# Kernel tuning notes

Hardware: AMD Instinct MI355X
Metric: run time of the kernel (lower is better)

## Reference

```python
import jax, jax.numpy as jnp
import numpy as np

B, S, D = 2, 2048, 1024
N_HEAD, D_ATTN = 16, 64


def setup_inputs() -> dict:
    key = jax.random.key(0)
    ks = jax.random.split(key, 5)
    x = jax.random.normal(ks[0], (B, S, D), dtype=jnp.float32)
    # causal mask: True = masked (as consumed by torch.masked_fill)
    mask = jnp.triu(jnp.ones((S, S), dtype=bool), k=1)
    scale = 0.02
    w_q = jax.random.normal(ks[1], (D, N_HEAD * D_ATTN), dtype=jnp.float32) * scale
    w_k = jax.random.normal(ks[2], (D, N_HEAD * D_ATTN), dtype=jnp.float32) * scale
    w_v = jax.random.normal(ks[3], (D, N_HEAD * D_ATTN), dtype=jnp.float32) * scale
    w_o = jax.random.normal(ks[4], (N_HEAD * D_ATTN, D), dtype=jnp.float32) * scale
    return {"x": x, "mask": mask, "w_q": w_q, "w_k": w_k, "w_v": w_v, "w_o": w_o}


def _split(t):
    # [B,S,H*Da] -> [B,H,S,Da]
    b, s, _ = t.shape
    return t.reshape(b, s, N_HEAD, D_ATTN).transpose(0, 2, 1, 3)


def reference(x, mask, w_q, w_k, w_v, w_o):
    q = _split(x @ w_q)
    k = _split(x @ w_k)
    v = _split(x @ w_v)
    scale = D_ATTN ** 0.5
    score = jnp.einsum("bhqd,bhkd->bhqk", q, k) / scale  # [B,H,S,S]
    score = jnp.where(mask, -jnp.inf, score)
    prob = jax.nn.softmax(score, axis=-1)
    out = jnp.einsum("bhqk,bhkd->bhqd", prob, v)
    out = out.transpose(0, 2, 1, 3).reshape(x.shape[0], x.shape[1], N_HEAD * D_ATTN)
    return out @ w_o
```

## Files before the change

kernel.cpp:

```cpp
#include <hip/hip_runtime.h>
#include <stdint.h>

using u16 = unsigned short;
using u32 = unsigned int;
using u64 = unsigned long long;

typedef float f32x4 __attribute__((ext_vector_type(4)));
typedef __bf16 bf16x8 __attribute__((ext_vector_type(8)));

#define DEV static __device__ __forceinline__

DEV u16 f2bf(float f) {
  u32 u = __float_as_uint(f);
  u += 0x7FFFu + ((u >> 16) & 1u);
  return (u16)(u >> 16);
}

DEV void gld16(const void* g, void* l) {
  __builtin_amdgcn_global_load_lds((__attribute__((address_space(1))) void*)g,
                                   (__attribute__((address_space(3))) void*)l,
                                   16, 0, 0);
}

__global__ void k_cvt_x(const float* __restrict__ x, u16* __restrict__ xb) {
  int i = (blockIdx.x * 256 + threadIdx.x) * 8;
  float4 a = *(const float4*)&x[i];
  float4 b = *(const float4*)&x[i + 4];
  __align__(16) u16 o[8];
  o[0] = f2bf(a.x); o[1] = f2bf(a.y); o[2] = f2bf(a.z); o[3] = f2bf(a.w);
  o[4] = f2bf(b.x); o[5] = f2bf(b.y); o[6] = f2bf(b.z); o[7] = f2bf(b.w);
  *(uint4*)&xb[i] = *(const uint4*)o;
}

__global__ void k_cvt_w(const float* __restrict__ w0, const float* __restrict__ w1,
                        const float* __restrict__ w2, const float* __restrict__ w3,
                        u16* __restrict__ t0, u16* __restrict__ t1,
                        u16* __restrict__ t2, u16* __restrict__ t3) {
  const float* w = blockIdx.z == 0 ? w0 : blockIdx.z == 1 ? w1 : blockIdx.z == 2 ? w2 : w3;
  u16* wt       = blockIdx.z == 0 ? t0 : blockIdx.z == 1 ? t1 : blockIdx.z == 2 ? t2 : t3;
  __shared__ __align__(16) float tile[64][68];
  const int tid = threadIdx.x;
  const int k0 = blockIdx.x * 64, n0 = blockIdx.y * 64;
#pragma unroll
  for (int i = 0; i < 4; ++i) {
    int c = tid + i * 256;
    int kr = c >> 4, col = (c & 15) * 4;
    *(float4*)&tile[kr][col] = *(const float4*)&w[(size_t)(k0 + kr) * 1024 + n0 + col];
  }
  __syncthreads();
#pragma unroll
  for (int i = 0; i < 2; ++i) {
    int c = tid + i * 256;
    int nr = c >> 3, kc = (c & 7) * 8;
    __align__(16) u16 o[8];
#pragma unroll
    for (int j = 0; j < 8; ++j) o[j] = f2bf(tile[kc + j][nr]);
    *(uint4*)&wt[(size_t)(n0 + nr) * 1024 + k0 + kc] = *(const uint4*)o;
  }
}

DEV void gemm_mainloop(const u16* __restrict__ A, const u16* __restrict__ Bt,
                       int m0, int n0, u16* Asb, u16* Bsb, f32x4 (&acc)[4][4]) {
  const int tid = threadIdx.x;
  const int lane = tid & 63;
  const int wv = tid >> 6;
  const int wm = (wv >> 1) * 64, wn = (wv & 1) * 64;

#pragma unroll
  for (int i = 0; i < 4; ++i)
#pragma unroll
    for (int j = 0; j < 4; ++j) {
      f32x4 z = {0.f, 0.f, 0.f, 0.f};
      acc[i][j] = z;
    }

  const int c0 = wv * 64 + lane, c1 = c0 + 256;
  const int r0 = c0 >> 2, r1 = c1 >> 2;
  const int b0 = (c0 & 3) ^ (r0 & 3) ^ ((r0 >> 2) & 3);
  const int b1 = (c1 & 3) ^ (r1 & 3) ^ ((r1 >> 2) & 3);
  const u16* ga0 = A + (size_t)(m0 + r0) * 1024 + b0 * 8;
  const u16* ga1 = A + (size_t)(m0 + r1) * 1024 + b1 * 8;
  const u16* gb0 = Bt + (size_t)(n0 + r0) * 1024 + b0 * 8;
  const u16* gb1 = Bt + (size_t)(n0 + r1) * 1024 + b1 * 8;
  u16* la0 = Asb + (wv * 64) * 8;
  u16* la1 = Asb + (wv * 64 + 256) * 8;
  u16* lb0 = Bsb + (wv * 64) * 8;
  u16* lb1 = Bsb + (wv * 64 + 256) * 8;

  int aoff[4], boff[4];
#pragma unroll
  for (int f = 0; f < 4; ++f) {
    int ra = wm + f * 16 + (lane & 15);
    aoff[f] = ra * 32 + (((lane >> 4) ^ (ra & 3) ^ ((ra >> 2) & 3)) * 8);
    int rb = wn + f * 16 + (lane & 15);
    boff[f] = rb * 32 + (((lane >> 4) ^ (rb & 3) ^ ((rb >> 2) & 3)) * 8);
  }

  for (int kt = 0; kt < 32; ++kt) {
    const int k0 = kt * 32;
    gld16(ga0 + k0, la0);
    gld16(ga1 + k0, la1);
    gld16(gb0 + k0, lb0);
    gld16(gb1 + k0, lb1);
    __syncthreads();
    bf16x8 af[4], bfv[4];
#pragma unroll
    for (int f = 0; f < 4; ++f) af[f] = *(const bf16x8*)&Asb[aoff[f]];
#pragma unroll
    for (int f = 0; f < 4; ++f) bfv[f] = *(const bf16x8*)&Bsb[boff[f]];
#pragma unroll
    for (int i = 0; i < 4; ++i)
#pragma unroll
      for (int j = 0; j < 4; ++j)
        acc[i][j] = __builtin_amdgcn_mfma_f32_16x16x32_bf16(af[i], bfv[j], acc[i][j], 0, 0, 0);
    __syncthreads();
  }
}

__global__ __launch_bounds__(256) void k_gemm_qkv(
    const u16* __restrict__ X, const u16* __restrict__ Wq, const u16* __restrict__ Wk,
    const u16* __restrict__ Wv, u16* __restrict__ Q, u16* __restrict__ K,
    u16* __restrict__ V) {
  __shared__ __align__(16) u16 Asb[128 * 32];
  __shared__ __align__(16) u16 Bsb[128 * 32];
  const int nb = blockIdx.x, mb = blockIdx.y;
  const int proj = nb >> 3, n0 = (nb & 7) * 128;
  const u16* W = proj == 0 ? Wq : proj == 1 ? Wk : Wv;
  u16* Dst = proj == 0 ? Q : proj == 1 ? K : V;
  const float scl = proj == 0 ? 0.125f * 1.4426950408889634f : 1.0f;
  f32x4 acc[4][4];
  gemm_mainloop(X, W, mb * 128, n0, Asb, Bsb, acc);
  const int lane = threadIdx.x & 63, wv = threadIdx.x >> 6;
  const int wm = (wv >> 1) * 64, wn = (wv & 1) * 64;
#pragma unroll
  for (int i = 0; i < 4; ++i)
#pragma unroll
    for (int j = 0; j < 4; ++j)
#pragma unroll
      for (int r = 0; r < 4; ++r) {
        int m = mb * 128 + wm + i * 16 + (lane >> 4) * 4 + r;
        int n = n0 + wn + j * 16 + (lane & 15);
        int b = m >> 11, s = m & 2047, h = n >> 6, d = n & 63;
        Dst[(size_t)((b * 16 + h) * 2048 + s) * 64 + d] = f2bf(acc[i][j][r] * scl);
      }
}

__global__ __launch_bounds__(256) void k_gemm_out(
    const u16* __restrict__ A, const u16* __restrict__ Wt, float* __restrict__ Out) {
  __shared__ __align__(16) u16 Asb[128 * 32];
  __shared__ __align__(16) u16 Bsb[128 * 32];
  const int nb = blockIdx.x, mb = blockIdx.y;
  f32x4 acc[4][4];
  gemm_mainloop(A, Wt, mb * 128, nb * 128, Asb, Bsb, acc);
  const int lane = threadIdx.x & 63, wv = threadIdx.x >> 6;
  const int wm = (wv >> 1) * 64, wn = (wv & 1) * 64;
#pragma unroll
  for (int i = 0; i < 4; ++i)
#pragma unroll
    for (int j = 0; j < 4; ++j)
#pragma unroll
      for (int r = 0; r < 4; ++r) {
        int m = mb * 128 + wm + i * 16 + (lane >> 4) * 4 + r;
        int n = nb * 128 + wn + j * 16 + (lane & 15);
        Out[(size_t)m * 1024 + n] = acc[i][j][r];
      }
}

__global__ void k_transpose_v(const u16* __restrict__ V, u16* __restrict__ Vt) {
  __shared__ __align__(16) u16 t[64][80];
  const int bh = blockIdx.y, s0 = blockIdx.x * 64;
  const int tid = threadIdx.x;
#pragma unroll
  for (int i = 0; i < 2; ++i) {
    int c = tid + i * 256;
    int sr = c >> 3, dc = (c & 7) * 8;
    *(uint4*)&t[sr][dc] = *(const uint4*)&V[((size_t)bh * 2048 + s0 + sr) * 64 + dc];
  }
  __syncthreads();
#pragma unroll
  for (int i = 0; i < 2; ++i) {
    int c = tid + i * 256;
    int dr = c >> 3, c7 = c & 7;
    __align__(8) u16 o[8];
#pragma unroll
    for (int j = 0; j < 8; ++j) o[j] = t[c7 * 8 + j][dr];
    int bp = ((c7 >> 1) & 1) * 32 + (c7 & 1) * 16 + ((c7 >> 2) & 1) * 4;
    u16* row = &Vt[((size_t)bh * 64 + dr) * 2048 + s0];
    *(u64*)&row[bp]     = *(const u64*)&o[0];
    *(u64*)&row[bp + 8] = *(const u64*)&o[4];
  }
}

__global__ __launch_bounds__(256) void k_attn(
    const u16* __restrict__ Qg, const u16* __restrict__ Kg,
    const u16* __restrict__ Vtg, u16* __restrict__ Og) {
  __shared__ __align__(16) u16 Ks[2][64 * 64];
  __shared__ __align__(16) u16 Vs[2][64 * 64];
  const int tid = threadIdx.x, lane = tid & 63, wv = tid >> 6;
  const int lo = lane & 15, hi = lane >> 4;
  const int jpair = blockIdx.x, bh = blockIdx.y;
  const u16* Qb = Qg + (size_t)bh * 2048 * 64;
  const u16* Kb = Kg + (size_t)bh * 2048 * 64;
  const u16* Vb = Vtg + (size_t)bh * 64 * 2048;
  const int b = bh >> 4, h = bh & 15;

  const int c0 = wv * 64 + lane, c1 = c0 + 256;
  const int r0 = c0 >> 3, r1 = c1 >> 3;
  const int e0 = ((c0 & 7) ^ (r0 & 7)) * 8;
  const int e1 = ((c1 & 7) ^ (r1 & 7)) * 8;

#pragma unroll 1
  for (int pass = 0; pass < 2; ++pass) {
    const int qt = pass == 0 ? jpair : 31 - jpair;
    const int q0 = qt * 64;
    const int nt = qt + 1;
    const int qq = q0 + wv * 16 + lo;

    bf16x8 qf[2];
#pragma unroll
    for (int kf = 0; kf < 2; ++kf)
      qf[kf] = *(const bf16x8*)&Qb[(size_t)(q0 + wv * 16 + lo) * 64 + kf * 32 + hi * 8];

    f32x4 ao[4];
#pragma unroll
    for (int df = 0; df < 4; ++df) {
      f32x4 z = {0.f, 0.f, 0.f, 0.f};
      ao[df] = z;
    }
    float m_run = -1e30f, l_run = 0.f;

    gld16(Kb + (size_t)r0 * 64 + e0, &Ks[0][wv * 512]);
    gld16(Kb + (size_t)r1 * 64 + e1, &Ks[0][wv * 512 + 2048]);
    gld16(Vb + (size_t)r0 * 2048 + e0, &Vs[0][wv * 512]);
    gld16(Vb + (size_t)r1 * 2048 + e1, &Vs[0][wv * 512 + 2048]);
    __syncthreads();

    int cur = 0;
#pragma unroll 1
    for (int t = 0; t < nt; ++t) {
      const int kv0 = t * 64;
      if (t + 1 < nt) {
        const int kn = kv0 + 64;
        gld16(Kb + (size_t)(kn + r0) * 64 + e0, &Ks[cur ^ 1][wv * 512]);
        gld16(Kb + (size_t)(kn + r1) * 64 + e1, &Ks[cur ^ 1][wv * 512 + 2048]);
        gld16(Vb + (size_t)r0 * 2048 + kn + e0, &Vs[cur ^ 1][wv * 512]);
        gld16(Vb + (size_t)r1 * 2048 + kn + e1, &Vs[cur ^ 1][wv * 512 + 2048]);
      }

      f32x4 sc[4];
#pragma unroll
      for (int cf = 0; cf < 4; ++cf) {
        f32x4 z = {0.f, 0.f, 0.f, 0.f};
        sc[cf] = z;
#pragma unroll
        for (int kf = 0; kf < 2; ++kf) {
          int row = cf * 16 + lo;
          int blk = ((kf * 4 + hi) ^ (row & 7)) * 8;
          bf16x8 kfr = *(const bf16x8*)&Ks[cur][row * 64 + blk];
          sc[cf] = __builtin_amdgcn_mfma_f32_16x16x32_bf16(kfr, qf[kf], sc[cf], 0, 0, 0);
        }
      }

      if (t == nt - 1) {
#pragma unroll
        for (int cf = 0; cf < 4; ++cf)
#pragma unroll
          for (int r = 0; r < 4; ++r) {
            int kk = kv0 + cf * 16 + hi * 4 + r;
            if (kk > qq) sc[cf][r] = -1e30f;
          }
      }

      float mx0 = fmaxf(fmaxf(sc[0][0], sc[0][1]), fmaxf(sc[0][2], sc[0][3]));
      float mx1 = fmaxf(fmaxf(sc[1][0], sc[1][1]), fmaxf(sc[1][2], sc[1][3]));
      float mx2 = fmaxf(fmaxf(sc[2][0], sc[2][1]), fmaxf(sc[2][2], sc[2][3]));
      float mx3 = fmaxf(fmaxf(sc[3][0], sc[3][1]), fmaxf(sc[3][2], sc[3][3]));
      float mx = fmaxf(fmaxf(mx0, mx1), fmaxf(mx2, mx3));
      mx = fmaxf(mx, __shfl_xor(mx, 16));
      mx = fmaxf(mx, __shfl_xor(mx, 32));

      if (__any(mx > m_run + 8.0f)) {
        float mnew = fmaxf(m_run, mx);
        float sclf = __builtin_amdgcn_exp2f(m_run - mnew);
        const int base = lane & 48;
#pragma unroll
        for (int r = 0; r < 4; ++r) {
          float s_r = __shfl(sclf, base + hi * 4 + r);
#pragma unroll
          for (int df = 0; df < 4; ++df) ao[df][r] *= s_r;
        }
        l_run *= sclf;
        m_run = mnew;
      }

      float pp[4];
      bf16x8 pa0, pa1;
#pragma unroll
      for (int cf = 0; cf < 4; ++cf) {
        float p0 = __builtin_amdgcn_exp2f(sc[cf][0] - m_run);
        float p1 = __builtin_amdgcn_exp2f(sc[cf][1] - m_run);
        float p2 = __builtin_amdgcn_exp2f(sc[cf][2] - m_run);
        float p3 = __builtin_amdgcn_exp2f(sc[cf][3] - m_run);
        pp[cf] = (p0 + p1) + (p2 + p3);
        bf16x8& pa = (cf & 1) ? pa1 : pa0;
        int j = (cf >> 1) * 4;
        pa[j] = (__bf16)p0; pa[j + 1] = (__bf16)p1;
        pa[j + 2] = (__bf16)p2; pa[j + 3] = (__bf16)p3;
      }
      float psum = (pp[0] + pp[1]) + (pp[2] + pp[3]);
      psum += __shfl_xor(psum, 16);
      psum += __shfl_xor(psum, 32);
      l_run += psum;

#pragma unroll
      for (int df = 0; df < 4; ++df) {
#pragma unroll
        for (int kf = 0; kf < 2; ++kf) {
          int row = df * 16 + lo;
          int blk = ((kf * 4 + hi) ^ (row & 7)) * 8;
          bf16x8 vfr = *(const bf16x8*)&Vs[cur][row * 64 + blk];
          ao[df] = __builtin_amdgcn_mfma_f32_16x16x32_bf16(kf == 0 ? pa0 : pa1, vfr,
                                                           ao[df], 0, 0, 0);
        }
      }
      __syncthreads();
      cur ^= 1;
    }

    float linv[4];
    const int base = lane & 48;
#pragma unroll
    for (int r = 0; r < 4; ++r) {
      float l_r = __shfl(l_run, base + hi * 4 + r);
      linv[r] = 1.0f / l_r;
    }
#pragma unroll
    for (int df = 0; df < 4; ++df)
#pragma unroll
      for (int r = 0; r < 4; ++r) {
        int s = q0 + wv * 16 + hi * 4 + r;
        int d = df * 16 + lo;
        Og[((size_t)(b * 2048 + s)) * 1024 + h * 64 + d] = f2bf(ao[df][r] * linv[r]);
      }
    __syncthreads();
  }
}

extern "C" void kernel_launch(void* const* d_in, const int* in_sizes, int n_in,
                              void* d_out, int out_size, void* d_ws, size_t ws_size,
                              hipStream_t stream) {
  const float* x = (const float*)d_in[0];
  const float* wq = (const float*)d_in[2];
  const float* wk = (const float*)d_in[3];
  const float* wv = (const float*)d_in[4];
  const float* wo = (const float*)d_in[5];

  char* ws = (char*)d_ws;
  u16* xb  = (u16*)(ws);
  u16* wqt = (u16*)(ws + 8388608);
  u16* wkt = (u16*)(ws + 8388608 + 2097152);
  u16* wvt = (u16*)(ws + 8388608 + 2 * 2097152);
  u16* wot = (u16*)(ws + 8388608 + 3 * 2097152);
  u16* qb  = (u16*)(ws + 16777216);
  u16* kb  = (u16*)(ws + 16777216 + 8388608);
  u16* vb  = (u16*)(ws + 16777216 + 2 * 8388608);
  u16* vt  = (u16*)(ws + 16777216 + 3 * 8388608);
  u16* ao  = (u16*)(ws + 16777216 + 4 * 8388608);

  k_cvt_x<<<dim3(2048), dim3(256), 0, stream>>>(x, xb);
  k_cvt_w<<<dim3(16, 16, 4), dim3(256), 0, stream>>>(wq, wk, wv, wo, wqt, wkt, wvt, wot);
  k_gemm_qkv<<<dim3(24, 32), dim3(256), 0, stream>>>(xb, wqt, wkt, wvt, qb, kb, vb);
  k_transpose_v<<<dim3(32, 32), dim3(256), 0, stream>>>(vb, vt);
  k_attn<<<dim3(16, 32), dim3(256), 0, stream>>>(qb, kb, vt, ao);
  k_gemm_out<<<dim3(8, 32), dim3(256), 0, stream>>>(ao, wot, (float*)d_out);
}
```

Measured before the change: 128.8 us.

## Process paired causal q-tiles concurrently in 512-thread blocks with shared K/V stream

The attention kernel now runs both q-tiles of a causal pair at the same time with 8 waves, instead of processing them in two sequential passes with 4 waves. The two halves share a single K/V tile stream, loaded once for the longer tile, so the shorter tile reuses the same loads and the total K/V traffic per block is reduced. Block indices are remapped so that heads are grouped per XCD for L2 locality, and s_setprio is raised around the MFMA sections. The cost is that waves for the shorter tile sit idle at barriers once their work is done, and each block needs more registers and threads.

```diff
diff --git a/kernel.cpp b/kernel.cpp
--- a/kernel.cpp
+++ b/kernel.cpp
@@ -191,77 +191,141 @@
   }
 }
 
-__global__ __launch_bounds__(256) void k_attn(
+DEV void qk_tile(const u16* Kc, const bf16x8 (&qf)[2], int lo, int hi, f32x4 (&sc)[4]) {
+#pragma unroll
+  for (int cf = 0; cf < 4; ++cf) {
+    f32x4 z = {0.f, 0.f, 0.f, 0.f};
+    sc[cf] = z;
+#pragma unroll
+    for (int kf = 0; kf < 2; ++kf) {
+      int row = cf * 16 + lo;
+      int blk = ((kf * 4 + hi) ^ (row & 7)) * 8;
+      bf16x8 kfr = *(const bf16x8*)&Kc[row * 64 + blk];
+      sc[cf] = __builtin_amdgcn_mfma_f32_16x16x32_bf16(kfr, qf[kf], sc[cf], 0, 0, 0);
+    }
+  }
+}
+
+DEV void sm_pv(f32x4 (&sc)[4], const u16* Vc, int lane, int lo, int hi,
+               float& m_run, float& l_run, f32x4 (&ao)[4]) {
+  float mx0 = fmaxf(fmaxf(sc[0][0], sc[0][1]), fmaxf(sc[0][2], sc[0][3]));
+  float mx1 = fmaxf(fmaxf(sc[1][0], sc[1][1]), fmaxf(sc[1][2], sc[1][3]));
+  float mx2 = fmaxf(fmaxf(sc[2][0], sc[2][1]), fmaxf(sc[2][2], sc[2][3]));
+  float mx3 = fmaxf(fmaxf(sc[3][0], sc[3][1]), fmaxf(sc[3][2], sc[3][3]));
+  float mx = fmaxf(fmaxf(mx0, mx1), fmaxf(mx2, mx3));
+  mx = fmaxf(mx, __shfl_xor(mx, 16));
+  mx = fmaxf(mx, __shfl_xor(mx, 32));
+
+  if (__any(mx > m_run + 8.0f)) {
+    float mnew = fmaxf(m_run, mx);
+    float sclf = __builtin_amdgcn_exp2f(m_run - mnew);
+    const int base = lane & 48;
+#pragma unroll
+    for (int r = 0; r < 4; ++r) {
+      float s_r = __shfl(sclf, base + hi * 4 + r);
+#pragma unroll
+      for (int df = 0; df < 4; ++df) ao[df][r] *= s_r;
+    }
+    l_run *= sclf;
+    m_run = mnew;
+  }
+
+  float pp[4];
+  bf16x8 pa0, pa1;
+#pragma unroll
+  for (int cf = 0; cf < 4; ++cf) {
+    float p0 = __builtin_amdgcn_exp2f(sc[cf][0] - m_run);
+    float p1 = __builtin_amdgcn_exp2f(sc[cf][1] - m_run);
+    float p2 = __builtin_amdgcn_exp2f(sc[cf][2] - m_run);
+    float p3 = __builtin_amdgcn_exp2f(sc[cf][3] - m_run);
+    pp[cf] = (p0 + p1) + (p2 + p3);
+    bf16x8& pa = (cf & 1) ? pa1 : pa0;
+    int j = (cf >> 1) * 4;
+    pa[j] = (__bf16)p0; pa[j + 1] = (__bf16)p1;
+    pa[j + 2] = (__bf16)p2; pa[j + 3] = (__bf16)p3;
+  }
+  float psum = (pp[0] + pp[1]) + (pp[2] + pp[3]);
+  psum += __shfl_xor(psum, 16);
+  psum += __shfl_xor(psum, 32);
+  l_run += psum;
+
+  __builtin_amdgcn_s_setprio(1);
+#pragma unroll
+  for (int df = 0; df < 4; ++df) {
+#pragma unroll
+    for (int kf = 0; kf < 2; ++kf) {
+      int row = df * 16 + lo;
+      int blk = ((kf * 4 + hi) ^ (row & 7)) * 8;
+      bf16x8 vfr = *(const bf16x8*)&Vc[row * 64 + blk];
+      ao[df] = __builtin_amdgcn_mfma_f32_16x16x32_bf16(kf == 0 ? pa0 : pa1, vfr,
+                                                       ao[df], 0, 0, 0);
+    }
+  }
+  __builtin_amdgcn_s_setprio(0);
+}
+
+__global__ __launch_bounds__(512) void k_attn(
     const u16* __restrict__ Qg, const u16* __restrict__ Kg,
     const u16* __restrict__ Vtg, u16* __restrict__ Og) {
   __shared__ __align__(16) u16 Ks[2][64 * 64];
   __shared__ __align__(16) u16 Vs[2][64 * 64];
   const int tid = threadIdx.x, lane = tid & 63, wv = tid >> 6;
   const int lo = lane & 15, hi = lane >> 4;
-  const int jpair = blockIdx.x, bh = blockIdx.y;
+  const int w4 = wv & 3, qsel = wv >> 2;
+
+  const int flat = blockIdx.y * 16 + blockIdx.x;
+  const int xcd = flat & 7, slot = flat >> 3;
+  const int bh = xcd * 4 + (slot >> 4);
+  const int jp = slot & 15;
+
   const u16* Qb = Qg + (size_t)bh * 2048 * 64;
   const u16* Kb = Kg + (size_t)bh * 2048 * 64;
   const u16* Vb = Vtg + (size_t)bh * 64 * 2048;
   const int b = bh >> 4, h = bh & 15;
 
-  const int c0 = wv * 64 + lane, c1 = c0 + 256;
-  const int r0 = c0 >> 3, r1 = c1 >> 3;
-  const int e0 = ((c0 & 7) ^ (r0 & 7)) * 8;
-  const int e1 = ((c1 & 7) ^ (r1 & 7)) * 8;
+  const int nta = jp + 1, ntb = 32 - jp;
+  const int q0 = (qsel ? (31 - jp) : jp) * 64;
+  const int myNt = qsel ? ntb : nta;
+  const int qq = q0 + w4 * 16 + lo;
+
+  bf16x8 qf[2];
+#pragma unroll
+  for (int kf = 0; kf < 2; ++kf)
+    qf[kf] = *(const bf16x8*)&Qb[(size_t)(q0 + w4 * 16 + lo) * 64 + kf * 32 + hi * 8];
+
+  f32x4 ao[4];
+#pragma unroll
+  for (int df = 0; df < 4; ++df) {
+    f32x4 z = {0.f, 0.f, 0.f, 0.f};
+    ao[df] = z;
+  }
+  float m_run = -1e30f, l_run = 0.f;
+
+  const int r0 = tid >> 3;
+  const int e0 = ((tid & 7) ^ (r0 & 7)) * 8;
+
+  gld16(Kb + (size_t)r0 * 64 + e0, &Ks[0][wv * 512]);
+  gld16(Vb + (size_t)r0 * 2048 + e0, &Vs[0][wv * 512]);
+  __syncthreads();
 
 #pragma unroll 1
-  for (int pass = 0; pass < 2; ++pass) {
-    const int qt = pass == 0 ? jpair : 31 - jpair;
-    const int q0 = qt * 64;
-    const int nt = qt + 1;
-    const int qq = q0 + wv * 16 + lo;
-
-    bf16x8 qf[2];
-#pragma unroll
-    for (int kf = 0; kf < 2; ++kf)
-      qf[kf] = *(const bf16x8*)&Qb[(size_t)(q0 + wv * 16 + lo) * 64 + kf * 32 + hi * 8];
-
-    f32x4 ao[4];
-#pragma unroll
-    for (int df = 0; df < 4; ++df) {
-      f32x4 z = {0.f, 0.f, 0.f, 0.f};
-      ao[df] = z;
-    }
-    float m_run = -1e30f, l_run = 0.f;
-
-    gld16(Kb + (size_t)r0 * 64 + e0, &Ks[0][wv * 512]);
-    gld16(Kb + (size_t)r1 * 64 + e1, &Ks[0][wv * 512 + 2048]);
-    gld16(Vb + (size_t)r0 * 2048 + e0, &Vs[0][wv * 512]);
-    gld16(Vb + (size_t)r1 * 2048 + e1, &Vs[0][wv * 512 + 2048]);
-    __syncthreads();
-
-    int cur = 0;
-#pragma unroll 1
-    for (int t = 0; t < nt; ++t) {
-      const int kv0 = t * 64;
-      if (t + 1 < nt) {
-        const int kn = kv0 + 64;
-        gld16(Kb + (size_t)(kn + r0) * 64 + e0, &Ks[cur ^ 1][wv * 512]);
-        gld16(Kb + (size_t)(kn + r1) * 64 + e1, &Ks[cur ^ 1][wv * 512 + 2048]);
-        gld16(Vb + (size_t)r0 * 2048 + kn + e0, &Vs[cur ^ 1][wv * 512]);
-        gld16(Vb + (size_t)r1 * 2048 + kn + e1, &Vs[cur ^ 1][wv * 512 + 2048]);
-      }
-
+  for (int t = 0; t < ntb; ++t) {
+    const u16* Kc = Ks[t & 1];
+    const u16* Vc = Vs[t & 1];
+    if (t + 1 < ntb) {
+      const int kn = (t + 1) * 64;
+      gld16(Kb + (size_t)(kn + r0) * 64 + e0, &Ks[(t + 1) & 1][wv * 512]);
+      gld16(Vb + (size_t)r0 * 2048 + kn + e0, &Vs[(t + 1) & 1][wv * 512]);
+    }
+
+    if (t < myNt) {
       f32x4 sc[4];
-#pragma unroll
-      for (int cf = 0; cf < 4; ++cf) {
-        f32x4 z = {0.f, 0.f, 0.f, 0.f};
-        sc[cf] = z;
-#pragma unroll
-        for (int kf = 0; kf < 2; ++kf) {
-          int row = cf * 16 + lo;
-          int blk = ((kf * 4 + hi) ^ (row & 7)) * 8;
-          bf16x8 kfr = *(const bf16x8*)&Ks[cur][row * 64 + blk];
-          sc[cf] = __builtin_amdgcn_mfma_f32_16x16x32_bf16(kfr, qf[kf], sc[cf], 0, 0, 0);
-        }
-      }
-
-      if (t == nt - 1) {
+      __builtin_amdgcn_s_setprio(1);
+      qk_tile(Kc, qf, lo, hi, sc);
+      __builtin_amdgcn_s_setprio(0);
+
+      if (t == myNt - 1) {
+        const int kv0 = t * 64;
 #pragma unroll
         for (int cf = 0; cf < 4; ++cf)
 #pragma unroll
@@ -271,79 +335,27 @@
           }
       }
 
-      float mx0 = fmaxf(fmaxf(sc[0][0], sc[0][1]), fmaxf(sc[0][2], sc[0][3]));
-      float mx1 = fmaxf(fmaxf(sc[1][0], sc[1][1]), fmaxf(sc[1][2], sc[1][3]));
-      float mx2 = fmaxf(fmaxf(sc[2][0], sc[2][1]), fmaxf(sc[2][2], sc[2][3]));
-      float mx3 = fmaxf(fmaxf(sc[3][0], sc[3][1]), fmaxf(sc[3][2], sc[3][3]));
-      float mx = fmaxf(fmaxf(mx0, mx1), fmaxf(mx2, mx3));
-      mx = fmaxf(mx, __shfl_xor(mx, 16));
-      mx = fmaxf(mx, __shfl_xor(mx, 32));
-
-      if (__any(mx > m_run + 8.0f)) {
-        float mnew = fmaxf(m_run, mx);
-        float sclf = __builtin_amdgcn_exp2f(m_run - mnew);
-        const int base = lane & 48;
-#pragma unroll
-        for (int r = 0; r < 4; ++r) {
-          float s_r = __shfl(sclf, base + hi * 4 + r);
-#pragma unroll
-          for (int df = 0; df < 4; ++df) ao[df][r] *= s_r;
-        }
-        l_run *= sclf;
-        m_run = mnew;
-      }
-
-      float pp[4];
-      bf16x8 pa0, pa1;
-#pragma unroll
-      for (int cf = 0; cf < 4; ++cf) {
-        float p0 = __builtin_amdgcn_exp2f(sc[cf][0] - m_run);
-        float p1 = __builtin_amdgcn_exp2f(sc[cf][1] - m_run);
-        float p2 = __builtin_amdgcn_exp2f(sc[cf][2] - m_run);
-        float p3 = __builtin_amdgcn_exp2f(sc[cf][3] - m_run);
-        pp[cf] = (p0 + p1) + (p2 + p3);
-        bf16x8& pa = (cf & 1) ? pa1 : pa0;
-        int j = (cf >> 1) * 4;
-        pa[j] = (__bf16)p0; pa[j + 1] = (__bf16)p1;
-        pa[j + 2] = (__bf16)p2; pa[j + 3] = (__bf16)p3;
-      }
-      float psum = (pp[0] + pp[1]) + (pp[2] + pp[3]);
-      psum += __shfl_xor(psum, 16);
-      psum += __shfl_xor(psum, 32);
-      l_run += psum;
-
-#pragma unroll
-      for (int df = 0; df < 4; ++df) {
-#pragma unroll
-        for (int kf = 0; kf < 2; ++kf) {
-          int row = df * 16 + lo;
-          int blk = ((kf * 4 + hi) ^ (row & 7)) * 8;
-          bf16x8 vfr = *(const bf16x8*)&Vs[cur][row * 64 + blk];
-          ao[df] = __builtin_amdgcn_mfma_f32_16x16x32_bf16(kf == 0 ? pa0 : pa1, vfr,
-                                                           ao[df], 0, 0, 0);
-        }
-      }
-      __syncthreads();
-      cur ^= 1;
-    }
-
-    float linv[4];
-    const int base = lane & 48;
+      sm_pv(sc, Vc, lane, lo, hi, m_run, l_run, ao);
+    }
+
+    __syncthreads();
+  }
+
+  float linv[4];
+  const int base = lane & 48;
+#pragma unroll
+  for (int r = 0; r < 4; ++r) {
+    float l_r = __shfl(l_run, base + hi * 4 + r);
+    linv[r] = 1.0f / l_r;
+  }
+#pragma unroll
+  for (int df = 0; df < 4; ++df)
 #pragma unroll
     for (int r = 0; r < 4; ++r) {
-      float l_r = __shfl(l_run, base + hi * 4 + r);
-      linv[r] = 1.0f / l_r;
-    }
-#pragma unroll
-    for (int df = 0; df < 4; ++df)
-#pragma unroll
-      for (int r = 0; r < 4; ++r) {
-        int s = q0 + wv * 16 + hi * 4 + r;
-        int d = df * 16 + lo;
-        Og[((size_t)(b * 2048 + s)) * 1024 + h * 64 + d] = f2bf(ao[df][r] * linv[r]);
-      }
-    __syncthreads();
-  }
+      int s = q0 + w4 * 16 + hi * 4 + r;
+      int d = df * 16 + lo;
+      Og[((size_t)(b * 2048 + s)) * 1024 + h * 64 + d] = f2bf(ao[df][r] * linv[r]);
+    }
 }
 
 extern "C" void kernel_launch(void* const* d_in, const int* in_sizes, int n_in,
@@ -371,6 +383,6 @@
   k_cvt_w<<<dim3(16, 16, 4), dim3(256), 0, stream>>>(wq, wk, wv, wo, wqt, wkt, wvt, wot);
   k_gemm_qkv<<<dim3(24, 32), dim3(256), 0, stream>>>(xb, wqt, wkt, wvt, qb, kb, vb);
   k_transpose_v<<<dim3(32, 32), dim3(256), 0, stream>>>(vb, vt);
-  k_attn<<<dim3(16, 32), dim3(256), 0, stream>>>(qb, kb, vt, ao);
+  k_attn<<<dim3(16, 32), dim3(512), 0, stream>>>(qb, kb, vt, ao);
   k_gemm_out<<<dim3(8, 32), dim3(256), 0, stream>>>(ao, wot, (float*)d_out);
 }
```

New measurement: 122.9 us. 1.05x faster.

## Split attention into one block per query tile with XCD-aware mapping; fuse conversion kernels

Applied to the files above, without the earlier changes.

The attention kernel now launches one block per query tile (1024 blocks) instead of pairing a short and a long tile inside one block. Block indices are remapped so that the heads sharing a K/V stream land on the same XCD, with mirrored tile orders to balance causal work. MFMA sections are wrapped in s_setprio so matrix work gets issue priority, and the x and weight conversion kernels are merged into one launch. This gives more parallelism and better L2 locality, but loses the built-in load balancing of pairing tiles and relies on the hardware dispatching blocks across XCDs round-robin.

```diff
diff --git a/kernel.cpp b/kernel.cpp
--- a/kernel.cpp
+++ b/kernel.cpp
@@ -22,36 +22,39 @@
                                    16, 0, 0);
 }
 
-__global__ void k_cvt_x(const float* __restrict__ x, u16* __restrict__ xb) {
-  int i = (blockIdx.x * 256 + threadIdx.x) * 8;
-  float4 a = *(const float4*)&x[i];
-  float4 b = *(const float4*)&x[i + 4];
-  __align__(16) u16 o[8];
-  o[0] = f2bf(a.x); o[1] = f2bf(a.y); o[2] = f2bf(a.z); o[3] = f2bf(a.w);
-  o[4] = f2bf(b.x); o[5] = f2bf(b.y); o[6] = f2bf(b.z); o[7] = f2bf(b.w);
-  *(uint4*)&xb[i] = *(const uint4*)o;
-}
-
-__global__ void k_cvt_w(const float* __restrict__ w0, const float* __restrict__ w1,
-                        const float* __restrict__ w2, const float* __restrict__ w3,
-                        u16* __restrict__ t0, u16* __restrict__ t1,
-                        u16* __restrict__ t2, u16* __restrict__ t3) {
-  const float* w = blockIdx.z == 0 ? w0 : blockIdx.z == 1 ? w1 : blockIdx.z == 2 ? w2 : w3;
-  u16* wt       = blockIdx.z == 0 ? t0 : blockIdx.z == 1 ? t1 : blockIdx.z == 2 ? t2 : t3;
+__global__ void k_cvt(const float* __restrict__ x, u16* __restrict__ xb,
+                      const float* __restrict__ w0, const float* __restrict__ w1,
+                      const float* __restrict__ w2, const float* __restrict__ w3,
+                      u16* __restrict__ t0, u16* __restrict__ t1,
+                      u16* __restrict__ t2, u16* __restrict__ t3) {
+  const int tid = threadIdx.x;
+  if (blockIdx.x < 2048) {
+    int i = (blockIdx.x * 256 + tid) * 8;
+    float4 a = *(const float4*)&x[i];
+    float4 b = *(const float4*)&x[i + 4];
+    __align__(16) u16 o[8];
+    o[0] = f2bf(a.x); o[1] = f2bf(a.y); o[2] = f2bf(a.z); o[3] = f2bf(a.w);
+    o[4] = f2bf(b.x); o[5] = f2bf(b.y); o[6] = f2bf(b.z); o[7] = f2bf(b.w);
+    *(uint4*)&xb[i] = *(const uint4*)o;
+    return;
+  }
+  const int c = blockIdx.x - 2048;
+  const int z = c >> 8, rem = c & 255;
+  const float* w = z == 0 ? w0 : z == 1 ? w1 : z == 2 ? w2 : w3;
+  u16* wt       = z == 0 ? t0 : z == 1 ? t1 : z == 2 ? t2 : t3;
   __shared__ __align__(16) float tile[64][68];
-  const int tid = threadIdx.x;
-  const int k0 = blockIdx.x * 64, n0 = blockIdx.y * 64;
+  const int k0 = (rem & 15) * 64, n0 = (rem >> 4) * 64;
 #pragma unroll
   for (int i = 0; i < 4; ++i) {
-    int c = tid + i * 256;
-    int kr = c >> 4, col = (c & 15) * 4;
+    int cc = tid + i * 256;
+    int kr = cc >> 4, col = (cc & 15) * 4;
     *(float4*)&tile[kr][col] = *(const float4*)&w[(size_t)(k0 + kr) * 1024 + n0 + col];
   }
   __syncthreads();
 #pragma unroll
   for (int i = 0; i < 2; ++i) {
-    int c = tid + i * 256;
-    int nr = c >> 3, kc = (c & 7) * 8;
+    int cc = tid + i * 256;
+    int nr = cc >> 3, kc = (cc & 7) * 8;
     __align__(16) u16 o[8];
 #pragma unroll
     for (int j = 0; j < 8; ++j) o[j] = f2bf(tile[kc + j][nr]);
@@ -191,6 +194,79 @@
   }
 }
 
+DEV void qk_tile(const u16* Kc, const bf16x8 (&qf)[2], int lo, int hi, f32x4 (&sc)[4]) {
+#pragma unroll
+  for (int cf = 0; cf < 4; ++cf) {
+    f32x4 z = {0.f, 0.f, 0.f, 0.f};
+    sc[cf] = z;
+#pragma unroll
+    for (int kf = 0; kf < 2; ++kf) {
+      int row = cf * 16 + lo;
+      int blk = ((kf * 4 + hi) ^ (row & 7)) * 8;
+      bf16x8 kfr = *(const bf16x8*)&Kc[row * 64 + blk];
+      sc[cf] = __builtin_amdgcn_mfma_f32_16x16x32_bf16(kfr, qf[kf], sc[cf], 0, 0, 0);
+    }
+  }
+}
+
+DEV void sm_pv(f32x4 (&sc)[4], const u16* Vc, int lane, int lo, int hi,
+               float& m_run, float& l_run, f32x4 (&ao)[4]) {
+  float mx0 = fmaxf(fmaxf(sc[0][0], sc[0][1]), fmaxf(sc[0][2], sc[0][3]));
+  float mx1 = fmaxf(fmaxf(sc[1][0], sc[1][1]), fmaxf(sc[1][2], sc[1][3]));
+  float mx2 = fmaxf(fmaxf(sc[2][0], sc[2][1]), fmaxf(sc[2][2], sc[2][3]));
+  float mx3 = fmaxf(fmaxf(sc[3][0], sc[3][1]), fmaxf(sc[3][2], sc[3][3]));
+  float mx = fmaxf(fmaxf(mx0, mx1), fmaxf(mx2, mx3));
+  mx = fmaxf(mx, __shfl_xor(mx, 16));
+  mx = fmaxf(mx, __shfl_xor(mx, 32));
+
+  if (__any(mx > m_run + 8.0f)) {
+    float mnew = fmaxf(m_run, mx);
+    float sclf = __builtin_amdgcn_exp2f(m_run - mnew);
+    const int base = lane & 48;
+#pragma unroll
+    for (int r = 0; r < 4; ++r) {
+      float s_r = __shfl(sclf, base + hi * 4 + r);
+#pragma unroll
+      for (int df = 0; df < 4; ++df) ao[df][r] *= s_r;
+    }
+    l_run *= sclf;
+    m_run = mnew;
+  }
+
+  float pp[4];
+  bf16x8 pa0, pa1;
+#pragma unroll
+  for (int cf = 0; cf < 4; ++cf) {
+    float p0 = __builtin_amdgcn_exp2f(sc[cf][0] - m_run);
+    float p1 = __builtin_amdgcn_exp2f(sc[cf][1] - m_run);
+    float p2 = __builtin_amdgcn_exp2f(sc[cf][2] - m_run);
+    float p3 = __builtin_amdgcn_exp2f(sc[cf][3] - m_run);
+    pp[cf] = (p0 + p1) + (p2 + p3);
+    bf16x8& pa = (cf & 1) ? pa1 : pa0;
+    int j = (cf >> 1) * 4;
+    pa[j] = (__bf16)p0; pa[j + 1] = (__bf16)p1;
+    pa[j + 2] = (__bf16)p2; pa[j + 3] = (__bf16)p3;
+  }
+  float psum = (pp[0] + pp[1]) + (pp[2] + pp[3]);
+  psum += __shfl_xor(psum, 16);
+  psum += __shfl_xor(psum, 32);
+  l_run += psum;
+
+  __builtin_amdgcn_s_setprio(1);
+#pragma unroll
+  for (int df = 0; df < 4; ++df) {
+#pragma unroll
+    for (int kf = 0; kf < 2; ++kf) {
+      int row = df * 16 + lo;
+      int blk = ((kf * 4 + hi) ^ (row & 7)) * 8;
+      bf16x8 vfr = *(const bf16x8*)&Vc[row * 64 + blk];
+      ao[df] = __builtin_amdgcn_mfma_f32_16x16x32_bf16(kf == 0 ? pa0 : pa1, vfr,
+                                                       ao[df], 0, 0, 0);
+    }
+  }
+  __builtin_amdgcn_s_setprio(0);
+}
+
 __global__ __launch_bounds__(256) void k_attn(
     const u16* __restrict__ Qg, const u16* __restrict__ Kg,
     const u16* __restrict__ Vtg, u16* __restrict__ Og) {
@@ -198,152 +274,97 @@
   __shared__ __align__(16) u16 Vs[2][64 * 64];
   const int tid = threadIdx.x, lane = tid & 63, wv = tid >> 6;
   const int lo = lane & 15, hi = lane >> 4;
-  const int jpair = blockIdx.x, bh = blockIdx.y;
+
+  const int flat = blockIdx.y * 32 + blockIdx.x;
+  const int xcd = flat & 7, slot = flat >> 3;
+  const int q4 = slot >> 5, cu = slot & 31;
+  const int bh = xcd * 4 + q4;
+  const int cux = (q4 & 2) ? (cu ^ 16) : cu;
+  const int qt = (q4 & 1) ? (31 - cux) : cux;
+
   const u16* Qb = Qg + (size_t)bh * 2048 * 64;
   const u16* Kb = Kg + (size_t)bh * 2048 * 64;
   const u16* Vb = Vtg + (size_t)bh * 64 * 2048;
   const int b = bh >> 4, h = bh & 15;
 
+  const int q0 = qt * 64;
+  const int nt = qt + 1;
+  const int qq = q0 + wv * 16 + lo;
+
+  bf16x8 qf[2];
+#pragma unroll
+  for (int kf = 0; kf < 2; ++kf)
+    qf[kf] = *(const bf16x8*)&Qb[(size_t)(q0 + wv * 16 + lo) * 64 + kf * 32 + hi * 8];
+
+  f32x4 ao[4];
+#pragma unroll
+  for (int df = 0; df < 4; ++df) {
+    f32x4 z = {0.f, 0.f, 0.f, 0.f};
+    ao[df] = z;
+  }
+  float m_run = -1e30f, l_run = 0.f;
+
   const int c0 = wv * 64 + lane, c1 = c0 + 256;
   const int r0 = c0 >> 3, r1 = c1 >> 3;
   const int e0 = ((c0 & 7) ^ (r0 & 7)) * 8;
   const int e1 = ((c1 & 7) ^ (r1 & 7)) * 8;
 
+  gld16(Kb + (size_t)r0 * 64 + e0, &Ks[0][wv * 512]);
+  gld16(Kb + (size_t)r1 * 64 + e1, &Ks[0][wv * 512 + 2048]);
+  gld16(Vb + (size_t)r0 * 2048 + e0, &Vs[0][wv * 512]);
+  gld16(Vb + (size_t)r1 * 2048 + e1, &Vs[0][wv * 512 + 2048]);
+  __syncthreads();
+
 #pragma unroll 1
-  for (int pass = 0; pass < 2; ++pass) {
-    const int qt = pass == 0 ? jpair : 31 - jpair;
-    const int q0 = qt * 64;
-    const int nt = qt + 1;
-    const int qq = q0 + wv * 16 + lo;
-
-    bf16x8 qf[2];
-#pragma unroll
-    for (int kf = 0; kf < 2; ++kf)
-      qf[kf] = *(const bf16x8*)&Qb[(size_t)(q0 + wv * 16 + lo) * 64 + kf * 32 + hi * 8];
-
-    f32x4 ao[4];
-#pragma unroll
-    for (int df = 0; df < 4; ++df) {
-      f32x4 z = {0.f, 0.f, 0.f, 0.f};
-      ao[df] = z;
-    }
-    float m_run = -1e30f, l_run = 0.f;
-
-    gld16(Kb + (size_t)r0 * 64 + e0, &Ks[0][wv * 512]);
-    gld16(Kb + (size_t)r1 * 64 + e1, &Ks[0][wv * 512 + 2048]);
-    gld16(Vb + (size_t)r0 * 2048 + e0, &Vs[0][wv * 512]);
-    gld16(Vb + (size_t)r1 * 2048 + e1, &Vs[0][wv * 512 + 2048]);
+  for (int t = 0; t < nt; ++t) {
+    const u16* Kc = Ks[t & 1];
+    const u16* Vc = Vs[t & 1];
+    if (t + 1 < nt) {
+      const int kn = (t + 1) * 64;
+      u16* kd = Ks[(t + 1) & 1];
+      u16* vd = Vs[(t + 1) & 1];
+      gld16(Kb + (size_t)(kn + r0) * 64 + e0, kd + wv * 512);
+      gld16(Kb + (size_t)(kn + r1) * 64 + e1, kd + wv * 512 + 2048);
+      gld16(Vb + (size_t)r0 * 2048 + kn + e0, vd + wv * 512);
+      gld16(Vb + (size_t)r1 * 2048 + kn + e1, vd + wv * 512 + 2048);
+    }
+
+    f32x4 sc[4];
+    __builtin_amdgcn_s_setprio(1);
+    qk_tile(Kc, qf, lo, hi, sc);
+    __builtin_amdgcn_s_setprio(0);
+
+    if (t == nt - 1) {
+      const int kv0 = t * 64;
+#pragma unroll
+      for (int cf = 0; cf < 4; ++cf)
+#pragma unroll
+        for (int r = 0; r < 4; ++r) {
+          int kk = kv0 + cf * 16 + hi * 4 + r;
+          if (kk > qq) sc[cf][r] = -1e30f;
+        }
+    }
+
+    sm_pv(sc, Vc, lane, lo, hi, m_run, l_run, ao);
+
     __syncthreads();
-
-    int cur = 0;
-#pragma unroll 1
-    for (int t = 0; t < nt; ++t) {
-      const int kv0 = t * 64;
-      if (t + 1 < nt) {
-        const int kn = kv0 + 64;
-        gld16(Kb + (size_t)(kn + r0) * 64 + e0, &Ks[cur ^ 1][wv * 512]);
-        gld16(Kb + (size_t)(kn + r1) * 64 + e1, &Ks[cur ^ 1][wv * 512 + 2048]);
-        gld16(Vb + (size_t)r0 * 2048 + kn + e0, &Vs[cur ^ 1][wv * 512]);
-        gld16(Vb + (size_t)r1 * 2048 + kn + e1, &Vs[cur ^ 1][wv * 512 + 2048]);
-      }
-
-      f32x4 sc[4];
-#pragma unroll
-      for (int cf = 0; cf < 4; ++cf) {
-        f32x4 z = {0.f, 0.f, 0.f, 0.f};
-        sc[cf] = z;
-#pragma unroll
-        for (int kf = 0; kf < 2; ++kf) {
-          int row = cf * 16 + lo;
-          int blk = ((kf * 4 + hi) ^ (row & 7)) * 8;
-          bf16x8 kfr = *(const bf16x8*)&Ks[cur][row * 64 + blk];
-          sc[cf] = __builtin_amdgcn_mfma_f32_16x16x32_bf16(kfr, qf[kf], sc[cf], 0, 0, 0);
-        }
-      }
-
-      if (t == nt - 1) {
-#pragma unroll
-        for (int cf = 0; cf < 4; ++cf)
-#pragma unroll
-          for (int r = 0; r < 4; ++r) {
-            int kk = kv0 + cf * 16 + hi * 4 + r;
-            if (kk > qq) sc[cf][r] = -1e30f;
-          }
-      }
-
-      float mx0 = fmaxf(fmaxf(sc[0][0], sc[0][1]), fmaxf(sc[0][2], sc[0][3]));
-      float mx1 = fmaxf(fmaxf(sc[1][0], sc[1][1]), fmaxf(sc[1][2], sc[1][3]));
-      float mx2 = fmaxf(fmaxf(sc[2][0], sc[2][1]), fmaxf(sc[2][2], sc[2][3]));
-      float mx3 = fmaxf(fmaxf(sc[3][0], sc[3][1]), fmaxf(sc[3][2], sc[3][3]));
-      float mx = fmaxf(fmaxf(mx0, mx1), fmaxf(mx2, mx3));
-      mx = fmaxf(mx, __shfl_xor(mx, 16));
-      mx = fmaxf(mx, __shfl_xor(mx, 32));
-
-      if (__any(mx > m_run + 8.0f)) {
-        float mnew = fmaxf(m_run, mx);
-        float sclf = __builtin_amdgcn_exp2f(m_run - mnew);
-        const int base = lane & 48;
-#pragma unroll
-        for (int r = 0; r < 4; ++r) {
-          float s_r = __shfl(sclf, base + hi * 4 + r);
-#pragma unroll
-          for (int df = 0; df < 4; ++df) ao[df][r] *= s_r;
-        }
-        l_run *= sclf;
-        m_run = mnew;
-      }
-
-      float pp[4];
-      bf16x8 pa0, pa1;
-#pragma unroll
-      for (int cf = 0; cf < 4; ++cf) {
-        float p0 = __builtin_amdgcn_exp2f(sc[cf][0] - m_run);
-        float p1 = __builtin_amdgcn_exp2f(sc[cf][1] - m_run);
-        float p2 = __builtin_amdgcn_exp2f(sc[cf][2] - m_run);
-        float p3 = __builtin_amdgcn_exp2f(sc[cf][3] - m_run);
-        pp[cf] = (p0 + p1) + (p2 + p3);
-        bf16x8& pa = (cf & 1) ? pa1 : pa0;
-        int j = (cf >> 1) * 4;
-        pa[j] = (__bf16)p0; pa[j + 1] = (__bf16)p1;
-        pa[j + 2] = (__bf16)p2; pa[j + 3] = (__bf16)p3;
-      }
-      float psum = (pp[0] + pp[1]) + (pp[2] + pp[3]);
-      psum += __shfl_xor(psum, 16);
-      psum += __shfl_xor(psum, 32);
-      l_run += psum;
-
-#pragma unroll
-      for (int df = 0; df < 4; ++df) {
-#pragma unroll
-        for (int kf = 0; kf < 2; ++kf) {
-          int row = df * 16 + lo;
-          int blk = ((kf * 4 + hi) ^ (row & 7)) * 8;
-          bf16x8 vfr = *(const bf16x8*)&Vs[cur][row * 64 + blk];
-          ao[df] = __builtin_amdgcn_mfma_f32_16x16x32_bf16(kf == 0 ? pa0 : pa1, vfr,
-                                                           ao[df], 0, 0, 0);
-        }
-      }
-      __syncthreads();
-      cur ^= 1;
-    }
-
-    float linv[4];
-    const int base = lane & 48;
+  }
+
+  float linv[4];
+  const int base = lane & 48;
+#pragma unroll
+  for (int r = 0; r < 4; ++r) {
+    float l_r = __shfl(l_run, base + hi * 4 + r);
+    linv[r] = 1.0f / l_r;
+  }
+#pragma unroll
+  for (int df = 0; df < 4; ++df)
 #pragma unroll
     for (int r = 0; r < 4; ++r) {
-      float l_r = __shfl(l_run, base + hi * 4 + r);
-      linv[r] = 1.0f / l_r;
-    }
-#pragma unroll
-    for (int df = 0; df < 4; ++df)
-#pragma unroll
-      for (int r = 0; r < 4; ++r) {
-        int s = q0 + wv * 16 + hi * 4 + r;
-        int d = df * 16 + lo;
-        Og[((size_t)(b * 2048 + s)) * 1024 + h * 64 + d] = f2bf(ao[df][r] * linv[r]);
-      }
-    __syncthreads();
-  }
+      int s = q0 + wv * 16 + hi * 4 + r;
+      int d = df * 16 + lo;
+      Og[((size_t)(b * 2048 + s)) * 1024 + h * 64 + d] = f2bf(ao[df][r] * linv[r]);
+    }
 }
 
 extern "C" void kernel_launch(void* const* d_in, const int* in_sizes, int n_in,
@@ -367,10 +388,9 @@
   u16* vt  = (u16*)(ws + 16777216 + 3 * 8388608);
   u16* ao  = (u16*)(ws + 16777216 + 4 * 8388608);
 
-  k_cvt_x<<<dim3(2048), dim3(256), 0, stream>>>(x, xb);
-  k_cvt_w<<<dim3(16, 16, 4), dim3(256), 0, stream>>>(wq, wk, wv, wo, wqt, wkt, wvt, wot);
+  k_cvt<<<dim3(3072), dim3(256), 0, stream>>>(x, xb, wq, wk, wv, wo, wqt, wkt, wvt, wot);
   k_gemm_qkv<<<dim3(24, 32), dim3(256), 0, stream>>>(xb, wqt, wkt, wvt, qb, kb, vb);
   k_transpose_v<<<dim3(32, 32), dim3(256), 0, stream>>>(vb, vt);
-  k_attn<<<dim3(16, 32), dim3(256), 0, stream>>>(qb, kb, vt, ao);
+  k_attn<<<dim3(32, 32), dim3(256), 0, stream>>>(qb, kb, vt, ao);
   k_gemm_out<<<dim3(8, 32), dim3(256), 0, stream>>>(ao, wot, (float*)d_out);
 }
```

After: 125.9 us. 2.3% less time.
